# Performance work log

Measured on AMD Instinct MI355X. Metric: run time of the kernel, lower is better.

Reference implementation:

```python
import jax, jax.numpy as jnp
import numpy as np

IN_CH = 256
NUM_CLASSES = 1
CONF_THR = 0.3
NMS_IOU = 0.2
ANCHOR_SIZES = (32.0, 64.0, 128.0)
ASPECTS = (0.5, 1.0, 2.0)
NUM_ANCHORS = len(ANCHOR_SIZES) * len(ASPECTS)  # 9
K_CAND = 1024   # top-score candidates fed to NMS per image
MAX_DET = 100   # max_output_size in source
BN_EPS = 1e-5


def _anchors():
    a = [[s * r / 224.0, s / r / 224.0] for s in ANCHOR_SIZES for r in ASPECTS]
    return jnp.asarray(a, jnp.float32)  # [A, 2] (w, h)


def _conv(x, w, b, pad):
    y = jax.lax.conv_general_dilated(x, w, (1, 1), [(pad, pad), (pad, pad)],
                                     dimension_numbers=('NCHW', 'OIHW', 'NCHW'))
    return y + b[None, :, None, None]


def _bn(x, g, b, m, v):
    inv = jax.lax.rsqrt(v + BN_EPS)
    return (x - m[None, :, None, None]) * (g * inv)[None, :, None, None] + b[None, :, None, None]


def _corners(b):
    return (b[..., 0] - b[..., 2] / 2, b[..., 1] - b[..., 3] / 2,
            b[..., 0] + b[..., 2] / 2, b[..., 1] + b[..., 3] / 2)


def _iou_one(box, boxes):
    # box: [4] cxcywh, boxes: [K,4] -> iou [K]
    ax1, ay1, ax2, ay2 = _corners(box)
    bx1, by1, bx2, by2 = _corners(boxes)
    iw = jnp.maximum(jnp.minimum(ax2, bx2) - jnp.maximum(ax1, bx1), 0.0)
    ih = jnp.maximum(jnp.minimum(ay2, by2) - jnp.maximum(ay1, by1), 0.0)
    inter = iw * ih
    union = (ax2 - ax1) * (ay2 - ay1) + (bx2 - bx1) * (by2 - by1) - inter
    return inter / (union + 1e-16)


def _nms(boxes, scores):
    # boxes [K,4], scores [K] -> kept boxes padded to [MAX_DET,4]
    s0 = jnp.where(scores > CONF_THR, scores, -1.0)

    def body(i, carry):
        s, out = carry
        j = jnp.argmax(s)
        ok = s[j] > 0.0
        box = boxes[j]
        iou = _iou_one(box, boxes)
        s_new = jnp.where(iou > NMS_IOU, -1.0, s).at[j].set(-1.0)
        s = jnp.where(ok, s_new, s)
        out = out.at[i].set(jnp.where(ok, box, jnp.zeros_like(box)))
        return s, out

    _, out = jax.lax.fori_loop(0, MAX_DET, body,
                               (s0, jnp.zeros((MAX_DET, 4), boxes.dtype)))
    return out


def _forward(features, w1, b1, g1, be1, m1, v1, w2, b2, g2, be2, m2, v2, wo, bo):
    x = jax.nn.relu(_bn(_conv(features, w1, b1, 1), g1, be1, m1, v1))
    x = jax.nn.relu(_bn(_conv(x, w2, b2, 1), g2, be2, m2, v2))
    p = _conv(x, wo, bo, 0)                      # [B, A*(5+C), H, W]
    B, _, H, W = p.shape
    p = p.reshape(B, NUM_ANCHORS, 5 + NUM_CLASSES, H, W).transpose(0, 3, 4, 1, 2)  # [B,H,W,A,5+C]
    obj = jax.nn.sigmoid(p[..., 4])
    anch = _anchors()
    gx = jnp.arange(W, dtype=p.dtype)[None, :, None]
    gy = jnp.arange(H, dtype=p.dtype)[:, None, None]
    px = (jax.nn.sigmoid(p[..., 0]) + gx) / W
    py = (jax.nn.sigmoid(p[..., 1]) + gy) / H
    pw = jnp.exp(p[..., 2]) * anch[:, 0]
    ph = jnp.exp(p[..., 3]) * anch[:, 1]
    boxes = jnp.stack([px, py, pw, ph], -1).reshape(B, -1, 4)
    if NUM_CLASSES > 1:
        scores = obj * jax.nn.sigmoid(p[..., 5:]).max(-1)
    else:
        scores = obj
    scores = scores.reshape(B, -1)

    def per_image(bx, sc):
        top_s, idx = jax.lax.top_k(sc, K_CAND)
        return _nms(bx[idx], top_s)

    return jax.vmap(per_image)(boxes, scores)    # [B, MAX_DET, 4]


def setup_inputs() -> dict:
    key = jax.random.key(0)
    ks = jax.random.split(key, 16)
    B = 32
    c1, c2 = IN_CH // 2, IN_CH // 4
    oc = NUM_ANCHORS * (5 + NUM_CLASSES)
    return {
        'features': jax.random.normal(ks[0], (B, IN_CH, 56, 56), jnp.float32),
        'w1': jax.random.normal(ks[1], (c1, IN_CH, 3, 3), jnp.float32) * 0.02,
        'b1': jax.random.normal(ks[2], (c1,), jnp.float32) * 0.02,
        'g1': 1.0 + 0.1 * jax.random.normal(ks[3], (c1,), jnp.float32),
        'be1': 0.1 * jax.random.normal(ks[4], (c1,), jnp.float32),
        'm1': 0.1 * jax.random.normal(ks[5], (c1,), jnp.float32),
        'v1': jax.random.uniform(ks[6], (c1,), jnp.float32, 0.5, 1.5),
        'w2': jax.random.normal(ks[7], (c2, c1, 3, 3), jnp.float32) * 0.03,
        'b2': jax.random.normal(ks[8], (c2,), jnp.float32) * 0.02,
        'g2': 1.0 + 0.1 * jax.random.normal(ks[9], (c2,), jnp.float32),
        'be2': 0.1 * jax.random.normal(ks[10], (c2,), jnp.float32),
        'm2': 0.1 * jax.random.normal(ks[11], (c2,), jnp.float32),
        'v2': jax.random.uniform(ks[12], (c2,), jnp.float32, 0.5, 1.5),
        'wo': jax.random.normal(ks[13], (oc, c2, 1, 1), jnp.float32) * 0.1,
        'bo': jax.random.normal(ks[14], (oc,), jnp.float32) * 0.05,
    }


def reference(features, w1, b1, g1, be1, m1, v1, w2, b2, g2, be2, m2, v2, wo, bo):
    return _forward(features, w1, b1, g1, be1, m1, v1, w2, b2, g2, be2, m2, v2, wo, bo)
```

## Files before the change

### kernel.cpp

```cpp
#include <hip/hip_runtime.h>
#include <math.h>

constexpr int BB   = 32;
constexpr int HW   = 3136;
constexpr int C0   = 256, C1 = 128, C2 = 64;
constexpr int NA   = 9;
constexpr int NCAND = HW * NA;
constexpr int KSEL  = 1024;
constexpr int MAXDET = 100;

typedef _Float16 half8 __attribute__((ext_vector_type(8)));
typedef _Float16 half4v __attribute__((ext_vector_type(4)));
typedef float    f32x4  __attribute__((ext_vector_type(4)));
typedef float    f32x16 __attribute__((ext_vector_type(16)));

__global__ void bn_prep(const float* __restrict__ g, const float* __restrict__ be,
                        const float* __restrict__ m, const float* __restrict__ v,
                        const float* __restrict__ cb,
                        float* __restrict__ scl, float* __restrict__ tb, int n) {
    int i = threadIdx.x;
    if (i < n) {
        float inv = 1.f / sqrtf(v[i] + 1e-5f);
        float s = g[i] * inv;
        scl[i] = s;
        tb[i] = be[i] + (cb[i] - m[i]) * s;
    }
}

__global__ void reorder_w6(const float* __restrict__ w, _Float16* __restrict__ wc,
                           int CIN, int COUT) {
    int i = blockIdx.x * 256 + threadIdx.x;
    int K = CIN * 9;
    if (i >= 2 * COUT * K) return;
    int ci  = i & 31;
    int row = (i >> 5) % (2 * COUT);
    int ch  = (i >> 5) / (2 * COUT);
    int pl  = row / COUT;
    int oc  = row - pl * COUT;
    int cg = ch / 9, r = ch - cg * 9;
    int cin = cg * 32 + ci;
    float v = w[oc * K + cin * 9 + r];
    _Float16 h = (_Float16)v;
    wc[i] = pl ? (_Float16)(v - (float)h) : h;
}

__global__ __launch_bounds__(256) void nchw_to_nhwc_split(
    const float* __restrict__ in, _Float16* __restrict__ hi, _Float16* __restrict__ lo)
{
    __shared__ float tile[64 * 68];
    const int pt = blockIdx.x * 64, ct = blockIdx.y * 64, b = blockIdx.z;
    const int t = threadIdx.x;
    const int r0 = t >> 4, cidx = (t & 15) * 4;
#pragma unroll
    for (int rr = 0; rr < 64; rr += 16) {
        int r = rr + r0;
        const float* src = in + ((size_t)(b * 256 + ct + r)) * HW + pt + cidx;
        float4 v = *(const float4*)src;
        float* d = &tile[r * 68 + cidx];
        d[0] = v.x; d[1] = v.y; d[2] = v.z; d[3] = v.w;
    }
    __syncthreads();
    const int p = t >> 2, c0 = (t & 3) * 16;
    size_t obase = ((size_t)(b * HW + pt + p)) * 256 + ct + c0;
    half8 h0, h1, l0, l1;
#pragma unroll
    for (int j = 0; j < 16; ++j) {
        float v = tile[(c0 + j) * 68 + p];
        _Float16 hh = (_Float16)v;
        _Float16 ll = (_Float16)(v - (float)hh);
        if (j < 8) { h0[j] = hh; l0[j] = ll; }
        else       { h1[j - 8] = hh; l1[j - 8] = ll; }
    }
    *(half8*)(hi + obase)     = h0;
    *(half8*)(hi + obase + 8) = h1;
    *(half8*)(lo + obase)     = l0;
    *(half8*)(lo + obase + 8) = l1;
}

template <int CIN, int COUT, int WAVES_P, bool NHWC_OUT>
__global__ __launch_bounds__(256, 2) void conv3x3_v9(
    const _Float16* __restrict__ xhi,
    const _Float16* __restrict__ xlo,
    const _Float16* __restrict__ wc,
    const float* __restrict__ scl, const float* __restrict__ tb,
    _Float16* __restrict__ ohi,
    _Float16* __restrict__ olo,
    float* __restrict__ onchw)
{
    constexpr int K     = CIN * 9;
    constexpr int NCH   = K / 32;
    constexpr int WAVES_O = 4 / WAVES_P;
    constexpr int PI    = 128 / (WAVES_P * 32);
    constexpr int WOC   = COUT / (WAVES_O * 32);
    constexpr int WROWS = 2 * COUT;
    constexpr int PROW  = 72;
    constexpr int WROW  = 40;
    constexpr int WLDS  = WROWS / 64;

    __shared__ _Float16 SP[2][128 * PROW];
    __shared__ _Float16 SW[2][WROWS * WROW];

    const int bid = blockIdx.x;
    const int swz = (bid & 7) * (gridDim.x >> 3) + (bid >> 3);
    const int b = swz / 25;
    const int pixBase = (swz - b * 25) * 128;
    const int bHW = b * HW;

    const int t = threadIdx.x;

    const int p     = t & 127;
    const int plane = t >> 7;
    const int pixA  = pixBase + p;
    const int ya = pixA / 56, xa = pixA - ya * 56;
    const bool pv = pixA < HW;
    const _Float16* xsrc = plane ? xlo : xhi;

    const int l = t & 63;
    const int wid = t >> 6;
    const int wp = wid % WAVES_P, wo = wid / WAVES_P;
    const int lc = l & 31, lk = l >> 5;

    f32x16 acc[PI][WOC];
#pragma unroll
    for (int pi = 0; pi < PI; ++pi)
#pragma unroll
        for (int oi = 0; oi < WOC; ++oi) acc[pi][oi] = (f32x16)0.f;

    auto issue = [&](int ch, half8 (&pld)[4], half8 (&wld)[WLDS]) {
        int cg = ch / 9, r = ch - cg * 9;
        int ky = r / 3, kx = r - ky * 3;
        int iy = ya + ky - 1, ix = xa + kx - 1;
        bool valid = pv && ((unsigned)iy < 56u) && ((unsigned)ix < 56u);
        int sp = pixA + (ky - 1) * 56 + (kx - 1);
        const _Float16* src = xsrc + (valid ? ((size_t)(bHW + sp)) * CIN + cg * 32 : 0);
#pragma unroll
        for (int q = 0; q < 4; ++q) pld[q] = *(const half8*)(src + q * 8);
        if (!valid) {
#pragma unroll
            for (int q = 0; q < 4; ++q)
#pragma unroll
                for (int j = 0; j < 8; ++j) pld[q][j] = (_Float16)0.f;
        }
        const _Float16* wsA = wc + (size_t)ch * WROWS * 32 + t * (WLDS * 8);
#pragma unroll
        for (int q = 0; q < WLDS; ++q) wld[q] = *(const half8*)(wsA + q * 8);
    };
    auto writeLDS = [&](int buf, half8 (&pld)[4], half8 (&wld)[WLDS]) {
#pragma unroll
        for (int q = 0; q < 4; ++q)
            *(half8*)&SP[buf][p * PROW + plane * 32 + q * 8] = pld[q];
#pragma unroll
        for (int q = 0; q < WLDS; ++q) {
            int h0 = t * (WLDS * 8) + q * 8;
            *(half8*)&SW[buf][(h0 >> 5) * WROW + (h0 & 31)] = wld[q];
        }
    };
    auto compute = [&](int buf) {
        __builtin_amdgcn_s_setprio(1);
#pragma unroll
        for (int ks = 0; ks < 2; ++ks) {
            half8 pb[PI][2];
#pragma unroll
            for (int pi = 0; pi < PI; ++pi) {
                int prw = wp * (PI * 32) + pi * 32 + lc;
#pragma unroll
                for (int pl2 = 0; pl2 < 2; ++pl2)
                    pb[pi][pl2] = *(const half8*)&SP[buf][prw * PROW + pl2 * 32 + ks * 16 + lk * 8];
            }
            half8 wa[WOC][2];
#pragma unroll
            for (int oi = 0; oi < WOC; ++oi)
#pragma unroll
                for (int pl2 = 0; pl2 < 2; ++pl2) {
                    int row = pl2 * COUT + wo * (WOC * 32) + oi * 32 + lc;
                    wa[oi][pl2] = *(const half8*)&SW[buf][row * WROW + ks * 16 + lk * 8];
                }
#pragma unroll
            for (int pi = 0; pi < PI; ++pi)
#pragma unroll
                for (int oi = 0; oi < WOC; ++oi) {
                    acc[pi][oi] = __builtin_amdgcn_mfma_f32_32x32x16_f16(wa[oi][0], pb[pi][0], acc[pi][oi], 0, 0, 0);
                    acc[pi][oi] = __builtin_amdgcn_mfma_f32_32x32x16_f16(wa[oi][0], pb[pi][1], acc[pi][oi], 0, 0, 0);
                    acc[pi][oi] = __builtin_amdgcn_mfma_f32_32x32x16_f16(wa[oi][1], pb[pi][0], acc[pi][oi], 0, 0, 0);
                }
        }
        __builtin_amdgcn_s_setprio(0);
    };

    half8 pA[4], wA[WLDS], pB[4], wB[WLDS];
    issue(0, pA, wA);
    writeLDS(0, pA, wA);
    issue(1, pB, wB);
    __syncthreads();

    for (int ch = 0; ch < NCH; ch += 2) {
        if (ch + 2 < NCH) issue(ch + 2, pA, wA);
        compute(0);
        writeLDS(1, pB, wB);
        __syncthreads();
        if (ch + 3 < NCH) issue(ch + 3, pB, wB);
        compute(1);
        if (ch + 2 < NCH) writeLDS(0, pA, wA);
        __syncthreads();
    }

#pragma unroll
    for (int pi = 0; pi < PI; ++pi) {
        const int pix = pixBase + wp * (PI * 32) + pi * 32 + lc;
        if (pix < HW) {
#pragma unroll
            for (int oi = 0; oi < WOC; ++oi) {
#pragma unroll
                for (int g = 0; g < 4; ++g) {
                    const int oc0 = wo * (WOC * 32) + oi * 32 + 8 * g + 4 * lk;
                    f32x4 s4 = *(const f32x4*)(scl + oc0);
                    f32x4 t4 = *(const f32x4*)(tb + oc0);
                    if constexpr (NHWC_OUT) {
                        half4v hh, ll;
#pragma unroll
                        for (int m2 = 0; m2 < 4; ++m2) {
                            float val = fmaxf(acc[pi][oi][g * 4 + m2] * s4[m2] + t4[m2], 0.f);
                            _Float16 h = (_Float16)val;
                            hh[m2] = h;
                            ll[m2] = (_Float16)(val - (float)h);
                        }
                        size_t o = ((size_t)(bHW + pix)) * COUT + oc0;
                        *(half4v*)(ohi + o) = hh;
                        *(half4v*)(olo + o) = ll;
                    } else {
#pragma unroll
                        for (int m2 = 0; m2 < 4; ++m2) {
                            float val = fmaxf(acc[pi][oi][g * 4 + m2] * s4[m2] + t4[m2], 0.f);
                            onchw[((size_t)(b * COUT + oc0 + m2)) * HW + pix] = val;
                        }
                    }
                }
            }
        }
    }
}

__global__ __launch_bounds__(256) void conv1x1_decode(
    const float* __restrict__ x2, const float* __restrict__ wo,
    const float* __restrict__ bo,
    float* __restrict__ boxes, float* __restrict__ scores)
{
    __shared__ float ws[64 * 56];
    for (int i = threadIdx.x; i < 54 * 64; i += 256) {
        int oc = i % 54, c = i / 54;
        ws[c * 56 + oc] = wo[oc * 64 + c];
    }
    __syncthreads();

    int u = blockIdx.x * 256 + threadIdx.x;
    int a = u % 9;
    int rest = u / 9;
    int quad = rest % 784;
    int b = rest / 784;
    int pix0 = quad * 4;
    int y = pix0 / 56;
    int x0 = pix0 - y * 56;

    const float* xb = x2 + (size_t)b * 64 * HW + pix0;
    float acc[5][4];
#pragma unroll
    for (int j = 0; j < 5; ++j)
#pragma unroll
        for (int p = 0; p < 4; ++p) acc[j][p] = 0.f;

#pragma unroll 8
    for (int c = 0; c < 64; ++c) {
        float4 xv = *(const float4*)(xb + c * HW);
#pragma unroll
        for (int j = 0; j < 5; ++j) {
            float w = ws[c * 56 + a * 6 + j];
            acc[j][0] += w * xv.x;
            acc[j][1] += w * xv.y;
            acc[j][2] += w * xv.z;
            acc[j][3] += w * xv.w;
        }
    }

    int si = a / 3, ri = a - si * 3;
    float sv = (float)(32 << si);
    float rv = 0.5f * (float)(1 << ri);
    float aw = (sv * rv) / 224.f;
    float ah = (sv / rv) / 224.f;
    float bo0 = bo[a * 6 + 0], bo1 = bo[a * 6 + 1], bo2 = bo[a * 6 + 2];
    float bo3 = bo[a * 6 + 3], bo4 = bo[a * 6 + 4];

#pragma unroll
    for (int p = 0; p < 4; ++p) {
        float p0 = acc[0][p] + bo0;
        float p1 = acc[1][p] + bo1;
        float p2 = acc[2][p] + bo2;
        float p3 = acc[3][p] + bo3;
        float p4 = acc[4][p] + bo4;
        float sx = 1.f / (1.f + expf(-p0));
        float sy = 1.f / (1.f + expf(-p1));
        float pxc = (sx + (float)(x0 + p)) / 56.f;
        float pyc = (sy + (float)y) / 56.f;
        float pw = expf(p2) * aw;
        float ph = expf(p3) * ah;
        float sc = 1.f / (1.f + expf(-p4));
        int n = (y * 56 + x0 + p) * 9 + a;
        float4 bx; bx.x = pxc; bx.y = pyc; bx.z = pw; bx.w = ph;
        *(float4*)&boxes[((size_t)b * NCAND + n) * 4] = bx;
        scores[(size_t)b * NCAND + n] = sc;
    }
}

__device__ __forceinline__ unsigned fkey(float f) {
    unsigned u = __float_as_uint(f);
    return (u & 0x80000000u) ? ~u : (u | 0x80000000u);
}

__global__ __launch_bounds__(1024) void topk_select(
    const float* __restrict__ scores, const float* __restrict__ boxes,
    float* __restrict__ cbox, float* __restrict__ csc, int* __restrict__ cidx)
{
    const int b = blockIdx.x, t = threadIdx.x;
    const float* sp = scores + (size_t)b * NCAND;
    const int lane = t & 63, w = t >> 6;

    __shared__ unsigned hist[256];
    __shared__ unsigned wsum[16];
    __shared__ unsigned s_sel, s_need, s_tot0, s_tot1;

    unsigned prefix = 0, maskSo = 0;
    int need = KSEL;

    for (int round = 0; round < 4; ++round) {
        int shift = 24 - round * 8;
        if (t < 256) hist[t] = 0;
        __syncthreads();
        for (int i = t; i < NCAND; i += 1024) {
            unsigned u = fkey(sp[i]);
            if ((u & maskSo) == prefix) atomicAdd(&hist[(u >> shift) & 255], 1u);
        }
        __syncthreads();
        if (t == 0) {
            int rem = need;
            unsigned sel = 0;
            for (int v = 255; v >= 0; --v) {
                int c = (int)hist[v];
                if (c >= rem) { sel = (unsigned)v; break; }
                rem -= c;
            }
            s_sel = sel; s_need = (unsigned)rem;
        }
        __syncthreads();
        prefix |= (s_sel << shift);
        maskSo |= (0xFFu << shift);
        need = (int)s_need;
        __syncthreads();
    }

    const unsigned cutoff = prefix;
    const unsigned needT = (unsigned)need;
    unsigned outBase = 0, tieBase = 0;
    const unsigned long long mlt = (1ull << lane) - 1ull;

    for (int c0 = 0; c0 < NCAND; c0 += 1024) {
        int i = c0 + t;
        bool valid = i < NCAND;
        float sc = valid ? sp[i] : 0.f;
        unsigned u = valid ? fkey(sc) : 0u;
        bool gt = valid && (u > cutoff);
        bool eq = valid && (u == cutoff);

        unsigned long long balE = __ballot(eq);
        unsigned lpE = (unsigned)__popcll(balE & mlt);
        if (lane == 0) wsum[w] = (unsigned)__popcll(balE);
        __syncthreads();
        if (t == 0) {
            unsigned run = 0;
            for (int k = 0; k < 16; ++k) { unsigned x = wsum[k]; wsum[k] = run; run += x; }
            s_tot1 = run;
        }
        __syncthreads();
        unsigned tieRank = tieBase + wsum[w] + lpE;
        bool take = gt || (eq && tieRank < needT);
        __syncthreads();

        unsigned long long balT = __ballot(take);
        unsigned lpT = (unsigned)__popcll(balT & mlt);
        if (lane == 0) wsum[w] = (unsigned)__popcll(balT);
        __syncthreads();
        if (t == 0) {
            unsigned run = 0;
            for (int k = 0; k < 16; ++k) { unsigned x = wsum[k]; wsum[k] = run; run += x; }
            s_tot0 = run;
        }
        __syncthreads();
        unsigned pos = outBase + wsum[w] + lpT;
        if (take) {
            float4 bx = *(const float4*)&boxes[((size_t)b * NCAND + i) * 4];
            *(float4*)&cbox[((size_t)b * KSEL + pos) * 4] = bx;
            csc[(size_t)b * KSEL + pos] = sc;
            cidx[(size_t)b * KSEL + pos] = i;
        }
        tieBase += s_tot1;
        outBase += s_tot0;
        __syncthreads();
    }
}

__global__ __launch_bounds__(64) void nms_wave(
    const float* __restrict__ cbox, const float* __restrict__ csc,
    const int* __restrict__ cidx, float* __restrict__ out)
{
    const int b = blockIdx.x, l = threadIdx.x;
    float cx[16], cy[16], w_[16], h_[16], s[16];
    int id[16];
#pragma unroll
    for (int j = 0; j < 16; ++j) {
        int ci = (b << 10) + (j << 6) + l;
        float4 bb = *(const float4*)&cbox[(size_t)ci * 4];
        float sc = csc[ci];
        cx[j] = bb.x; cy[j] = bb.y; w_[j] = bb.z; h_[j] = bb.w;
        s[j] = sc > 0.3f ? sc : -1.f;
        id[j] = cidx[ci];
    }
    float* ob = out + (size_t)b * MAXDET * 4;

    for (int it = 0; it < MAXDET; ++it) {
        float bs = s[0]; int bi = id[0];
        float bcx = cx[0], bcy = cy[0], bw = w_[0], bh = h_[0];
#pragma unroll
        for (int j = 1; j < 16; ++j) {
            bool tk = (s[j] > bs) || (s[j] == bs && id[j] < bi);
            if (tk) { bs = s[j]; bi = id[j]; bcx = cx[j]; bcy = cy[j]; bw = w_[j]; bh = h_[j]; }
        }
#pragma unroll
        for (int m2 = 1; m2 < 64; m2 <<= 1) {
            float os = __shfl_xor(bs, m2); int oi = __shfl_xor(bi, m2);
            float ox = __shfl_xor(bcx, m2), oy = __shfl_xor(bcy, m2);
            float ow = __shfl_xor(bw, m2), oh2 = __shfl_xor(bh, m2);
            bool tk = (os > bs) || (os == bs && oi < bi);
            if (tk) { bs = os; bi = oi; bcx = ox; bcy = oy; bw = ow; bh = oh2; }
        }
        if (bs <= 0.f) {
            for (int q = it * 4 + l; q < MAXDET * 4; q += 64) ob[q] = 0.f;
            break;
        }
        if (l == 0) {
            float4 o; o.x = bcx; o.y = bcy; o.z = bw; o.w = bh;
            *(float4*)&ob[it * 4] = o;
        }
        float wx1 = bcx - bw / 2.f, wy1 = bcy - bh / 2.f;
        float wx2 = bcx + bw / 2.f, wy2 = bcy + bh / 2.f;
        float war = (wx2 - wx1) * (wy2 - wy1);
#pragma unroll
        for (int j = 0; j < 16; ++j) {
            float jx1 = cx[j] - w_[j] / 2.f, jy1 = cy[j] - h_[j] / 2.f;
            float jx2 = cx[j] + w_[j] / 2.f, jy2 = cy[j] + h_[j] / 2.f;
            float iw = fminf(wx2, jx2) - fmaxf(wx1, jx1); iw = fmaxf(iw, 0.f);
            float ih = fminf(wy2, jy2) - fmaxf(wy1, jy1); ih = fmaxf(ih, 0.f);
            float inter = iw * ih;
            float jar = (jx2 - jx1) * (jy2 - jy1);
            float uni = war + jar - inter;
            if (inter / (uni + 1e-16f) > 0.2f) s[j] = -1.f;
        }
    }
}

extern "C" void kernel_launch(void* const* d_in, const int* in_sizes, int n_in,
                              void* d_out, int out_size, void* d_ws, size_t ws_size,
                              hipStream_t stream)
{
    const float* features = (const float*)d_in[0];
    const float* w1 = (const float*)d_in[1];
    const float* b1 = (const float*)d_in[2];
    const float* g1 = (const float*)d_in[3];
    const float* be1 = (const float*)d_in[4];
    const float* m1 = (const float*)d_in[5];
    const float* v1 = (const float*)d_in[6];
    const float* w2 = (const float*)d_in[7];
    const float* b2 = (const float*)d_in[8];
    const float* g2 = (const float*)d_in[9];
    const float* be2 = (const float*)d_in[10];
    const float* m2 = (const float*)d_in[11];
    const float* v2 = (const float*)d_in[12];
    const float* wo = (const float*)d_in[13];
    const float* bo = (const float*)d_in[14];

    char* ws = (char*)d_ws;
    size_t off = 0;
    auto alloc = [&](size_t bytes) {
        char* p = ws + off;
        off += (bytes + 255) / 256 * 256;
        return p;
    };

    _Float16* w1c = (_Float16*)alloc((size_t)2 * C1 * 2304 * 2);
    _Float16* w2c = (_Float16*)alloc((size_t)2 * C2 * 1152 * 2);
    float* scl1 = (float*)alloc(C1 * 4);
    float* tb1  = (float*)alloc(C1 * 4);
    float* scl2 = (float*)alloc(C2 * 4);
    float* tb2  = (float*)alloc(C2 * 4);

    const size_t planeF = (size_t)BB * HW * C0 * 2;
    char* regB = alloc(2 * planeF);
    _Float16* fhi = (_Float16*)regB;
    _Float16* flo = (_Float16*)(regB + planeF);

    const size_t planeX1 = (size_t)BB * HW * C1 * 2;
    char* regC = alloc(2 * planeX1);
    _Float16* x1hi = (_Float16*)regC;
    _Float16* x1lo = (_Float16*)(regC + planeX1);

    float* x2     = (float*)regB;
    float* boxes  = (float*)(regB + 25690112);
    float* scores = (float*)(regB + 25690112 + 14450688);
    float* cbox = (float*)regC;
    float* csc  = (float*)(regC + 524288);
    int*   cidx = (int*)(regC + 524288 + 131072);

    bn_prep<<<1, 256, 0, stream>>>(g1, be1, m1, v1, b1, scl1, tb1, C1);
    bn_prep<<<1, 256, 0, stream>>>(g2, be2, m2, v2, b2, scl2, tb2, C2);
    reorder_w6<<<(2 * C1 * 2304 + 255) / 256, 256, 0, stream>>>(w1, w1c, C0, C1);
    reorder_w6<<<(2 * C2 * 1152 + 255) / 256, 256, 0, stream>>>(w2, w2c, C1, C2);

    nchw_to_nhwc_split<<<dim3(49, 4, BB), 256, 0, stream>>>(features, fhi, flo);

    conv3x3_v9<C0, C1, 2, true><<<800, 256, 0, stream>>>(
        fhi, flo, w1c, scl1, tb1, x1hi, x1lo, nullptr);
    conv3x3_v9<C1, C2, 4, false><<<800, 256, 0, stream>>>(
        x1hi, x1lo, w2c, scl2, tb2, nullptr, nullptr, x2);

    conv1x1_decode<<<(BB * 784 * NA) / 256, 256, 0, stream>>>(x2, wo, bo, boxes, scores);

    topk_select<<<BB, 1024, 0, stream>>>(scores, boxes, cbox, csc, cidx);
    nms_wave<<<BB, 64, 0, stream>>>(cbox, csc, cidx, (float*)d_out);
}
```

Baseline: 691.0 us.

## Stage conv tiles via direct global-to-LDS loads with XOR swizzle, single buffer

Replaces the register-staged double-buffered LDS pipeline in the 3x3 conv kernels with direct global_load_lds DMA into a single XOR-swizzled shared tile. Out-of-bounds pixels read from a zeroed scratch buffer. The aim is to free VGPRs and LDS so that four blocks fit per CU. The cost is that the load/compute overlap within a block is lost, since each chunk is now stage, sync, compute, sync. Overlap then has to come from higher occupancy instead.

```diff
diff --git a/kernel.cpp b/kernel.cpp
--- a/kernel.cpp
+++ b/kernel.cpp
@@ -1,5 +1,6 @@
 #include <hip/hip_runtime.h>
 #include <math.h>
+#include <stdint.h>
 
 constexpr int BB   = 32;
 constexpr int HW   = 3136;
@@ -13,6 +14,14 @@
 typedef _Float16 half4v __attribute__((ext_vector_type(4)));
 typedef float    f32x4  __attribute__((ext_vector_type(4)));
 typedef float    f32x16 __attribute__((ext_vector_type(16)));
+
+__device__ __forceinline__ void g2l16(const void* g, void* l) {
+    auto gp = reinterpret_cast<const __attribute__((address_space(1))) char*>(
+        reinterpret_cast<uintptr_t>(g));
+    auto lp = reinterpret_cast<__attribute__((address_space(3))) char*>(
+        reinterpret_cast<uintptr_t>(l));
+    __builtin_amdgcn_global_load_lds(gp, lp, 16, 0, 0);
+}
 
 __global__ void bn_prep(const float* __restrict__ g, const float* __restrict__ be,
                         const float* __restrict__ m, const float* __restrict__ v,
@@ -77,28 +86,27 @@
     *(half8*)(lo + obase + 8) = l1;
 }
 
-template <int CIN, int COUT, int WAVES_P, bool NHWC_OUT>
-__global__ __launch_bounds__(256, 2) void conv3x3_v9(
+template <int CIN, int COUT, int MINW, bool NHWC_OUT>
+__global__ __launch_bounds__(256, MINW) void conv3x3_v10(
     const _Float16* __restrict__ xhi,
     const _Float16* __restrict__ xlo,
     const _Float16* __restrict__ wc,
+    const _Float16* __restrict__ zbuf,
     const float* __restrict__ scl, const float* __restrict__ tb,
     _Float16* __restrict__ ohi,
     _Float16* __restrict__ olo,
     float* __restrict__ onchw)
 {
-    constexpr int K     = CIN * 9;
-    constexpr int NCH   = K / 32;
-    constexpr int WAVES_O = 4 / WAVES_P;
-    constexpr int PI    = 128 / (WAVES_P * 32);
-    constexpr int WOC   = COUT / (WAVES_O * 32);
-    constexpr int WROWS = 2 * COUT;
-    constexpr int PROW  = 72;
-    constexpr int WROW  = 40;
-    constexpr int WLDS  = WROWS / 64;
-
-    __shared__ _Float16 SP[2][128 * PROW];
-    __shared__ _Float16 SW[2][WROWS * WROW];
+    constexpr int K       = CIN * 9;
+    constexpr int NCH     = K / 32;
+    constexpr int WROWS   = 2 * COUT;
+    constexpr int CHALVES = WROWS * 32;
+    constexpr int WI      = WROWS / 64;
+    constexpr int PI      = 2;
+    constexpr int WOC     = COUT / 64;
+
+    __shared__ __align__(16) _Float16 SP[128 * 64];
+    __shared__ __align__(16) _Float16 SW[WROWS * 32];
 
     const int bid = blockIdx.x;
     const int swz = (bid & 7) * (gridDim.x >> 3) + (bid >> 3);
@@ -106,18 +114,25 @@
     const int pixBase = (swz - b * 25) * 128;
     const int bHW = b * HW;
 
-    const int t = threadIdx.x;
-
-    const int p     = t & 127;
-    const int plane = t >> 7;
-    const int pixA  = pixBase + p;
-    const int ya = pixA / 56, xa = pixA - ya * 56;
-    const bool pv = pixA < HW;
-    const _Float16* xsrc = plane ? xlo : xhi;
-
-    const int l = t & 63;
+    const int t = threadIdx.x, l = t & 63, w = t >> 6;
+
+    const int cpix = (l & 7) ^ ((l >> 3) & 7);
+    const int ppl = cpix >> 2, pq = cpix & 3;
+    const _Float16* xsp = ppl ? xlo : xhi;
+    int py[4], px[4];
+    const _Float16* pbase[4];
+#pragma unroll
+    for (int i = 0; i < 4; ++i) {
+        int p = w * 32 + i * 8 + (l >> 3);
+        int pix = pixBase + p;
+        py[i] = pix / 56; px[i] = pix - py[i] * 56;
+        pbase[i] = xsp + (size_t)(bHW + pix) * CIN + pq * 8;
+    }
+    const int cw = (l & 3) ^ ((l >> 3) & 3);
+    const _Float16* wbase = wc + ((size_t)(w * (WI * 16) + (l >> 2))) * 32 + cw * 8;
+
     const int wid = t >> 6;
-    const int wp = wid % WAVES_P, wo = wid / WAVES_P;
+    const int wp = wid & 1, wo = wid >> 1;
     const int lc = l & 31, lk = l >> 5;
 
     f32x16 acc[PI][WOC];
@@ -126,46 +141,36 @@
 #pragma unroll
         for (int oi = 0; oi < WOC; ++oi) acc[pi][oi] = (f32x16)0.f;
 
-    auto issue = [&](int ch, half8 (&pld)[4], half8 (&wld)[WLDS]) {
+    auto stage = [&](int ch) {
         int cg = ch / 9, r = ch - cg * 9;
-        int ky = r / 3, kx = r - ky * 3;
-        int iy = ya + ky - 1, ix = xa + kx - 1;
-        bool valid = pv && ((unsigned)iy < 56u) && ((unsigned)ix < 56u);
-        int sp = pixA + (ky - 1) * 56 + (kx - 1);
-        const _Float16* src = xsrc + (valid ? ((size_t)(bHW + sp)) * CIN + cg * 32 : 0);
-#pragma unroll
-        for (int q = 0; q < 4; ++q) pld[q] = *(const half8*)(src + q * 8);
-        if (!valid) {
-#pragma unroll
-            for (int q = 0; q < 4; ++q)
-#pragma unroll
-                for (int j = 0; j < 8; ++j) pld[q][j] = (_Float16)0.f;
-        }
-        const _Float16* wsA = wc + (size_t)ch * WROWS * 32 + t * (WLDS * 8);
-#pragma unroll
-        for (int q = 0; q < WLDS; ++q) wld[q] = *(const half8*)(wsA + q * 8);
+        int ky = r / 3;
+        int dy = ky - 1, dx = (r - ky * 3) - 1;
+        int off = (dy * 56 + dx) * CIN + cg * 32;
+#pragma unroll
+        for (int i = 0; i < 4; ++i) {
+            bool v = ((unsigned)(py[i] + dy) < 56u) && ((unsigned)(px[i] + dx) < 56u);
+            const void* src = v ? (const void*)(pbase[i] + off) : (const void*)zbuf;
+            g2l16(src, (void*)&SP[w * 2048 + i * 512]);
+        }
+        const _Float16* wsrc = wbase + (size_t)ch * CHALVES;
+#pragma unroll
+        for (int j = 0; j < WI; ++j)
+            g2l16((const void*)(wsrc + j * 512), (void*)&SW[(w * WI + j) * 512]);
     };
-    auto writeLDS = [&](int buf, half8 (&pld)[4], half8 (&wld)[WLDS]) {
-#pragma unroll
-        for (int q = 0; q < 4; ++q)
-            *(half8*)&SP[buf][p * PROW + plane * 32 + q * 8] = pld[q];
-#pragma unroll
-        for (int q = 0; q < WLDS; ++q) {
-            int h0 = t * (WLDS * 8) + q * 8;
-            *(half8*)&SW[buf][(h0 >> 5) * WROW + (h0 & 31)] = wld[q];
-        }
-    };
-    auto compute = [&](int buf) {
-        __builtin_amdgcn_s_setprio(1);
+
+    auto compute = [&]() {
 #pragma unroll
         for (int ks = 0; ks < 2; ++ks) {
             half8 pb[PI][2];
 #pragma unroll
             for (int pi = 0; pi < PI; ++pi) {
                 int prw = wp * (PI * 32) + pi * 32 + lc;
-#pragma unroll
-                for (int pl2 = 0; pl2 < 2; ++pl2)
-                    pb[pi][pl2] = *(const half8*)&SP[buf][prw * PROW + pl2 * 32 + ks * 16 + lk * 8];
+                int key = prw & 7;
+#pragma unroll
+                for (int pl2 = 0; pl2 < 2; ++pl2) {
+                    int c = pl2 * 4 + ks * 2 + lk;
+                    pb[pi][pl2] = *(const half8*)&SP[prw * 64 + ((c ^ key) << 3)];
+                }
             }
             half8 wa[WOC][2];
 #pragma unroll
@@ -173,7 +178,8 @@
 #pragma unroll
                 for (int pl2 = 0; pl2 < 2; ++pl2) {
                     int row = pl2 * COUT + wo * (WOC * 32) + oi * 32 + lc;
-                    wa[oi][pl2] = *(const half8*)&SW[buf][row * WROW + ks * 16 + lk * 8];
+                    int c = ks * 2 + lk;
+                    wa[oi][pl2] = *(const half8*)&SW[row * 32 + ((c ^ ((row >> 1) & 3)) << 3)];
                 }
 #pragma unroll
             for (int pi = 0; pi < PI; ++pi)
@@ -184,23 +190,12 @@
                     acc[pi][oi] = __builtin_amdgcn_mfma_f32_32x32x16_f16(wa[oi][1], pb[pi][0], acc[pi][oi], 0, 0, 0);
                 }
         }
-        __builtin_amdgcn_s_setprio(0);
     };
 
-    half8 pA[4], wA[WLDS], pB[4], wB[WLDS];
-    issue(0, pA, wA);
-    writeLDS(0, pA, wA);
-    issue(1, pB, wB);
-    __syncthreads();
-
-    for (int ch = 0; ch < NCH; ch += 2) {
-        if (ch + 2 < NCH) issue(ch + 2, pA, wA);
-        compute(0);
-        writeLDS(1, pB, wB);
-        __syncthreads();
-        if (ch + 3 < NCH) issue(ch + 3, pB, wB);
-        compute(1);
-        if (ch + 2 < NCH) writeLDS(0, pA, wA);
+    for (int ch = 0; ch < NCH; ++ch) {
+        stage(ch);
+        __syncthreads();
+        compute();
         __syncthreads();
     }
 
@@ -493,6 +488,7 @@
         return p;
     };
 
+    _Float16* zbuf = (_Float16*)alloc(256);
     _Float16* w1c = (_Float16*)alloc((size_t)2 * C1 * 2304 * 2);
     _Float16* w2c = (_Float16*)alloc((size_t)2 * C2 * 1152 * 2);
     float* scl1 = (float*)alloc(C1 * 4);
@@ -517,6 +513,7 @@
     float* csc  = (float*)(regC + 524288);
     int*   cidx = (int*)(regC + 524288 + 131072);
 
+    hipMemsetAsync(zbuf, 0, 256, stream);
     bn_prep<<<1, 256, 0, stream>>>(g1, be1, m1, v1, b1, scl1, tb1, C1);
     bn_prep<<<1, 256, 0, stream>>>(g2, be2, m2, v2, b2, scl2, tb2, C2);
     reorder_w6<<<(2 * C1 * 2304 + 255) / 256, 256, 0, stream>>>(w1, w1c, C0, C1);
@@ -524,10 +521,10 @@
 
     nchw_to_nhwc_split<<<dim3(49, 4, BB), 256, 0, stream>>>(features, fhi, flo);
 
-    conv3x3_v9<C0, C1, 2, true><<<800, 256, 0, stream>>>(
-        fhi, flo, w1c, scl1, tb1, x1hi, x1lo, nullptr);
-    conv3x3_v9<C1, C2, 4, false><<<800, 256, 0, stream>>>(
-        x1hi, x1lo, w2c, scl2, tb2, nullptr, nullptr, x2);
+    conv3x3_v10<C0, C1, 4, true><<<800, 256, 0, stream>>>(
+        fhi, flo, w1c, zbuf, scl1, tb1, x1hi, x1lo, nullptr);
+    conv3x3_v10<C1, C2, 4, false><<<800, 256, 0, stream>>>(
+        x1hi, x1lo, w2c, zbuf, scl2, tb2, nullptr, nullptr, x2);
 
     conv1x1_decode<<<(BB * 784 * NA) / 256, 256, 0, stream>>>(x2, wo, bo, boxes, scores);
 
```

Result: faster. 650.1 us (-5.9%).
